# Kernel optimization log

Hardware: AMD Instinct MI355X
Metric: run time of the kernel (lower is better)

The kernel has to match this reference:

```python
import jax, jax.numpy as jnp
import numpy as np

# Module hyperparameters (from init_kwargs)
IN_C = 64
OUT_C = 64
K = 3
STRIDE = 1
PAD = 1
DIL = 1
OVERLAP = 4
CENTER_SIZE = 4

# Input sizes
B, H, W = 16, 128, 128


def _crop_mask(h, w):
    """Static (trace-time) crop mask: zeros on the central crop window, ones elsewhere.

    Matches the intended semantics of CropConv's python-loop mask: rows
    [crop_start, crop_start+crop_size) x cols [crop_start, crop_start+crop_size)
    of the HxW output grid are zeroed.
    """
    crop_start = (h - h // CENTER_SIZE) // 2 - OVERLAP  # 44 for h=128
    crop_size = h // CENTER_SIZE + 2 * OVERLAP          # 40 for h=128
    m = np.ones((h, w), dtype=np.float32)
    m[crop_start:crop_start + crop_size, crop_start:crop_start + crop_size] = 0.0
    return jnp.asarray(m)


def setup_inputs() -> dict:
    key = jax.random.key(0)
    kx, kw = jax.random.split(key)
    x = jax.random.normal(kx, (B, IN_C, H, W), dtype=jnp.float32)
    # kaiming_normal_ fan_out init: std = sqrt(2 / (out_channels * k * k))
    w_std = np.sqrt(2.0 / (OUT_C * K * K)).astype(np.float32)
    weight = jax.random.normal(kw, (OUT_C, IN_C, K, K), dtype=jnp.float32) * w_std
    return {"x": x, "weight": weight}


def reference(x, weight):
    # im2col (Unfold) + matmul == a standard dense conv; use the fused conv primitive.
    out = jax.lax.conv_general_dilated(
        x, weight,
        window_strides=(STRIDE, STRIDE),
        padding=((PAD, PAD), (PAD, PAD)),
        rhs_dilation=(DIL, DIL),
        dimension_numbers=("NCHW", "OIHW", "NCHW"),
    )  # [B, OUT_C, H, W] (same-size conv)
    mask = _crop_mask(out.shape[2], out.shape[3])  # [H, W], {0,1}
    # torch.where(mask, out, 0) == out * mask (mask is constant wrt grads)
    return out * mask
```

## Files before the change

kernel.cpp:

```cpp
#include <hip/hip_runtime.h>
#include <stdint.h>


#define B_ 16
#define C_ 64
#define H_ 128
#define W_ 128

#define TCOLS_A 130
#define XLDS_A (3 * TCOLS_A * 8)

typedef float f32x4 __attribute__((ext_vector_type(4)));
typedef short bf16x8 __attribute__((ext_vector_type(8)));

__device__ inline unsigned short f2bf(float f) {
    union { float f; uint32_t u; } v; v.f = f;
    uint32_t u = v.u + 0x7FFF + ((v.u >> 16) & 1);
    return (unsigned short)(u >> 16);
}

__global__ __launch_bounds__(256) void xform_weight(
    const float* __restrict__ wgt, uint16_t* __restrict__ Wb)
{
    int L = blockIdx.x * 256 + threadIdx.x;
    int e    = L & 7;
    int lane = (L >> 3) & 63;
    int i    = (L >> 9) & 3;
    int ch   = (L >> 11) & 1;
    int kk   = L >> 12;
    int oc   = i * 16 + (lane & 15);
    int ic   = ch * 32 + (lane >> 4) * 8 + e;
    Wb[L] = f2bf(wgt[((size_t)oc * 64 + ic) * 9 + kk]);
}

__global__ __launch_bounds__(256, 2) void conv_main(
    const uint4* __restrict__ Wq,
    const float* __restrict__ x,
    float* __restrict__ out)
{
    __shared__ uint4 lds[XLDS_A];

    const int t    = threadIdx.x;
    const int lane = t & 63;
    const int wv   = t >> 6;
    const int n    = lane & 15;
    const int q    = lane >> 4;

    const int d    = blockIdx.x;
    const int orig = (d & 7) * 256 + (d >> 3);
    const int ht   = orig & 127;
    const int b    = orig >> 7;

    const int ohalf = wv & 1;
    const int wq    = (wv >> 1) * 64;

    bf16x8 Areg[18][2];
    #pragma unroll
    for (int g = 0; g < 18; ++g)
        #pragma unroll
        for (int i = 0; i < 2; ++i)
            Areg[g][i] = __builtin_bit_cast(bf16x8,
                Wq[(g * 4 + ohalf * 2 + i) * 64 + lane]);

    {
        const int j     = t & 7;
        const int c4    = t >> 3;
        const int cbase = 1 + c4 * 4;
        const int wg0   = c4 * 4;

        #pragma unroll
        for (int r = 0; r < 3; ++r) {
            const int h = ht - 1 + r;
            if (h < 0 || h >= H_) {
                uint4 z; z.x = z.y = z.z = z.w = 0;
                #pragma unroll
                for (int cc = 0; cc < 4; ++cc)
                    lds[(r * TCOLS_A + cbase + cc) * 8 +
                        ((j + cbase + cc) & 7)] = z;
            } else {
                const float* src =
                    x + (((size_t)(b * C_ + j * 8)) * H_ + h) * W_ + wg0;
                f32x4 f[8];
                #pragma unroll
                for (int e = 0; e < 8; ++e)
                    f[e] = *(const f32x4*)(src + (size_t)e * (H_ * W_));
                #pragma unroll
                for (int cc = 0; cc < 4; ++cc) {
                    uint32_t u[4];
                    #pragma unroll
                    for (int p = 0; p < 4; ++p)
                        u[p] = (uint32_t)f2bf(f[2 * p][cc]) |
                               ((uint32_t)f2bf(f[2 * p + 1][cc]) << 16);
                    lds[(r * TCOLS_A + cbase + cc) * 8 +
                        ((j + cbase + cc) & 7)] = *(const uint4*)u;
                }
            }
        }
        if (t < 48) {
            const int ce = (t < 24) ? 0 : (TCOLS_A - 1);
            const int u  = (t < 24) ? t : t - 24;
            const int r  = u >> 3, jj = u & 7;
            uint4 z; z.x = z.y = z.z = z.w = 0;
            lds[(r * TCOLS_A + ce) * 8 + ((jj + ce) & 7)] = z;
        }
    }
    __syncthreads();

    f32x4 acc[2][4];
    #pragma unroll
    for (int i = 0; i < 2; ++i)
        #pragma unroll
        for (int f = 0; f < 4; ++f)
            acc[i][f] = (f32x4){0.f, 0.f, 0.f, 0.f};

    #pragma unroll
    for (int kh = 0; kh < 3; ++kh) {
        #pragma unroll
        for (int kw = 0; kw < 3; ++kw) {
            #pragma unroll
            for (int ch = 0; ch < 2; ++ch) {
                const int g = (kh * 3 + kw) * 2 + ch;
                bf16x8 bb[4];
                #pragma unroll
                for (int f = 0; f < 4; ++f) {
                    const int ct  = wq + f * 16 + n + kw;
                    const int idx = (kh * TCOLS_A + ct) * 8 +
                                    ((ch * 4 + q + ct) & 7);
                    bb[f] = __builtin_bit_cast(bf16x8, lds[idx]);
                }
                #pragma unroll
                for (int i = 0; i < 2; ++i)
                    #pragma unroll
                    for (int f = 0; f < 4; ++f)
                        acc[i][f] = __builtin_amdgcn_mfma_f32_16x16x32_bf16(
                            Areg[g][i], bb[f], acc[i][f], 0, 0, 0);
            }
        }
    }

    const int  h  = ht;
    const bool hz = (h >= 44 && h < 84);
    #pragma unroll
    for (int f = 0; f < 4; ++f) {
        const int w0 = wq + f * 16 + n;
        const bool zz = hz && (w0 >= 44 && w0 < 84);
        #pragma unroll
        for (int i = 0; i < 2; ++i) {
            #pragma unroll
            for (int r = 0; r < 4; ++r) {
                const int oc = ohalf * 32 + i * 16 + q * 4 + r;
                out[(((size_t)b * C_ + oc) * H_ + h) * W_ + w0] =
                    zz ? 0.f : acc[i][f][r];
            }
        }
    }
}

#define WLDS_U4 4608
#define FXLDS_U4 4096

__global__ __launch_bounds__(256, 1) void conv_fused(
    const float* __restrict__ x,
    const float* __restrict__ wgt,
    float* __restrict__ out)
{
    __shared__ uint4 lds[WLDS_U4 + FXLDS_U4];
    uint16_t* lds16 = (uint16_t*)lds;

    const int t    = threadIdx.x;
    const int lane = t & 63;
    const int wv   = t >> 6;
    const int n    = lane & 15;
    const int q    = lane >> 4;

    const int d    = blockIdx.x;
    const int orig = (d & 7) * 128 + (d >> 3);
    const int b    = orig >> 6;
    const int h0   = (orig & 63) * 2;

    #pragma unroll
    for (int p = 0; p < 2; ++p) {
        const int a_  = t + 256 * p;
        const int oc  = a_ >> 3;
        const int oct = a_ & 7;
        const float* src = wgt + (size_t)oc * 576 + (size_t)oct * 72;
        f32x4 w4[18];
        #pragma unroll
        for (int j = 0; j < 18; ++j) w4[j] = ((const f32x4*)src)[j];
        const int ch = oct >> 2, qq = oct & 3;
        const int ii = oc >> 4,  nn = oc & 15;
        #pragma unroll
        for (int kk = 0; kk < 9; ++kk) {
            #define WELEM(e) ((uint32_t)f2bf(w4[((e)*9 + kk) >> 2][((e)*9 + kk) & 3]))
            uint4 val;
            val.x = WELEM(0) | (WELEM(1) << 16);
            val.y = WELEM(2) | (WELEM(3) << 16);
            val.z = WELEM(4) | (WELEM(5) << 16);
            val.w = WELEM(6) | (WELEM(7) << 16);
            #undef WELEM
            lds[((kk * 2 + ch) * 4 + ii) * 64 + qq * 16 + nn] = val;
        }
    }

    {
        const int ic    = t >> 2;
        const int w0    = (t & 3) * 32;
        const int jslot = ic >> 3;
        const int esub  = ic & 7;
        #pragma unroll
        for (int r = 0; r < 4; ++r) {
            const int h = h0 - 1 + r;
            if (h < 0 || h >= H_) {
                uint4 z; z.x = z.y = z.z = z.w = 0;
                #pragma unroll
                for (int k = 0; k < 4; ++k)
                    lds[WLDS_U4 + r * 1024 + k * 256 + t] = z;
            } else {
                const float* src =
                    x + (((size_t)(b * C_ + ic)) * H_ + h) * W_ + w0;
                f32x4 v4[8];
                #pragma unroll
                for (int j = 0; j < 8; ++j) v4[j] = ((const f32x4*)src)[j];
                #pragma unroll
                for (int k = 0; k < 32; ++k) {
                    const int c    = w0 + k;
                    const int slot = (jslot + c) & 7;
                    lds16[WLDS_U4 * 8 + ((r * 128 + c) * 8 + slot) * 8 + esub] =
                        f2bf(v4[k >> 2][k & 3]);
                }
            }
        }
    }
    __syncthreads();

    f32x4 acc[4][4];
    #pragma unroll
    for (int i = 0; i < 4; ++i)
        #pragma unroll
        for (int tt = 0; tt < 4; ++tt)
            acc[i][tt] = (f32x4){0.f, 0.f, 0.f, 0.f};

    const int wb = (wv & 1) * 64;
    const uint4* Wl = lds;
    const uint4* Xl = lds + WLDS_U4;
    const bool lz = (wb + n) == 0;
    const bool rz = (wb + n) == 79;
    const bf16x8 zfrag = 0;

    #pragma unroll
    for (int kh = 0; kh < 3; ++kh) {
        const int row = (wv >> 1) + kh;
        #pragma unroll
        for (int kw = 0; kw < 3; ++kw) {
            const int kk = kh * 3 + kw;
            #pragma unroll
            for (int ch = 0; ch < 2; ++ch) {
                bf16x8 a[4], bb[4];
                #pragma unroll
                for (int i = 0; i < 4; ++i)
                    a[i] = __builtin_bit_cast(bf16x8,
                        Wl[((kk * 2 + ch) * 4 + i) * 64 + lane]);
                #pragma unroll
                for (int tt = 0; tt < 4; ++tt) {
                    int c   = wb + tt * 16 + n + kw - 1;
                    int cc  = min(max(c, 0), 127);
                    int idx = (row * 128 + cc) * 8 + ((ch * 4 + q + cc) & 7);
                    bf16x8 v = __builtin_bit_cast(bf16x8, Xl[idx]);
                    if (kw == 0 && tt == 0) v = lz ? zfrag : v;
                    if (kw == 2 && tt == 3) v = rz ? zfrag : v;
                    bb[tt] = v;
                }
                #pragma unroll
                for (int i = 0; i < 4; ++i)
                    #pragma unroll
                    for (int tt = 0; tt < 4; ++tt)
                        acc[i][tt] = __builtin_amdgcn_mfma_f32_16x16x32_bf16(
                            a[i], bb[tt], acc[i][tt], 0, 0, 0);
            }
        }
    }

    const int  h  = h0 + (wv >> 1);
    const bool hz = (h >= 44 && h < 84);
    #pragma unroll
    for (int i = 0; i < 4; ++i) {
        #pragma unroll
        for (int tt = 0; tt < 4; ++tt) {
            const int  w0 = wb + tt * 16 + n;
            const bool zz = hz && (w0 >= 44 && w0 < 84);
            #pragma unroll
            for (int r = 0; r < 4; ++r) {
                const int oc = i * 16 + q * 4 + r;
                out[(((size_t)b * C_ + oc) * H_ + h) * W_ + w0] =
                    zz ? 0.f : acc[i][tt][r];
            }
        }
    }
}

extern "C" void kernel_launch(void* const* d_in, const int* in_sizes, int n_in,
                              void* d_out, int out_size, void* d_ws, size_t ws_size,
                              hipStream_t stream) {
    const float* x   = (const float*)d_in[0];
    const float* wgt = (const float*)d_in[1];
    float* out       = (float*)d_out;

    const size_t W_BYTES = 9 * 2 * 4 * 64 * 16;
    if (ws_size >= W_BYTES) {
        uint16_t* Wb = (uint16_t*)d_ws;
        xform_weight<<<dim3(144), dim3(256), 0, stream>>>(wgt, Wb);
        conv_main<<<dim3(2048), dim3(256), 0, stream>>>(
            (const uint4*)Wb, x, out);
    } else {
        conv_fused<<<dim3(1024), dim3(256), 0, stream>>>(x, wgt, out);
    }
}
```

Measured before the change: 138.9 us.

## Process four output rows per block with a rotating LDS row ring and prefetch

Each block now computes four consecutive output rows instead of one, keeping a 4-slot ring of input rows in LDS so each new row needs only one extra row load instead of three. The next row's global loads are issued before the MFMA loop and written to LDS afterwards, overlapping memory latency with compute. This reduces redundant input reads and weight register reloads, but cuts the grid from 2048 to 512 blocks, which lowers parallelism and occupancy slack, and adds per-iteration barriers.

```diff
diff --git a/kernel.cpp b/kernel.cpp
--- a/kernel.cpp
+++ b/kernel.cpp
@@ -8,7 +8,9 @@
 #define W_ 128
 
 #define TCOLS_A 130
-#define XLDS_A (3 * TCOLS_A * 8)
+#define ROWU4   (TCOLS_A * 8)
+#define XLDS_R  (4 * ROWU4)
+#define T_TILES 4
 
 typedef float f32x4 __attribute__((ext_vector_type(4)));
 typedef short bf16x8 __attribute__((ext_vector_type(8)));
@@ -33,12 +35,51 @@
     Wb[L] = f2bf(wgt[((size_t)oc * 64 + ic) * 9 + kk]);
 }
 
+__device__ __forceinline__ void stage_row_now(
+    uint4* lds, const float* __restrict__ xb, int p, int t)
+{
+    const int j     = t & 7;
+    const int c4    = t >> 3;
+    const int cbase = 1 + c4 * 4;
+    const int wg0   = c4 * 4;
+    const int sb    = (p & 3) * ROWU4;
+    const int h     = p - 1;
+    if (h < 0 || h >= H_) {
+        uint4 z; z.x = z.y = z.z = z.w = 0;
+        #pragma unroll
+        for (int cc = 0; cc < 4; ++cc)
+            lds[sb + (cbase + cc) * 8 + ((j + cbase + cc) & 7)] = z;
+    } else {
+        const float* src = xb + ((size_t)(j * 8) * H_ + h) * W_ + wg0;
+        f32x4 f[8];
+        #pragma unroll
+        for (int e = 0; e < 8; ++e)
+            f[e] = *(const f32x4*)(src + (size_t)e * (H_ * W_));
+        #pragma unroll
+        for (int cc = 0; cc < 4; ++cc) {
+            uint32_t u[4];
+            #pragma unroll
+            for (int pp = 0; pp < 4; ++pp)
+                u[pp] = (uint32_t)f2bf(f[2 * pp][cc]) |
+                        ((uint32_t)f2bf(f[2 * pp + 1][cc]) << 16);
+            lds[sb + (cbase + cc) * 8 + ((j + cbase + cc) & 7)] =
+                *(const uint4*)u;
+        }
+    }
+    if (t < 16) {
+        const int ce = (t < 8) ? 0 : (TCOLS_A - 1);
+        const int jj = t & 7;
+        uint4 z; z.x = z.y = z.z = z.w = 0;
+        lds[sb + ce * 8 + ((jj + ce) & 7)] = z;
+    }
+}
+
 __global__ __launch_bounds__(256, 2) void conv_main(
     const uint4* __restrict__ Wq,
     const float* __restrict__ x,
     float* __restrict__ out)
 {
-    __shared__ uint4 lds[XLDS_A];
+    __shared__ uint4 lds[XLDS_R];
 
     const int t    = threadIdx.x;
     const int lane = t & 63;
@@ -47,12 +88,15 @@
     const int q    = lane >> 4;
 
     const int d    = blockIdx.x;
-    const int orig = (d & 7) * 256 + (d >> 3);
-    const int ht   = orig & 127;
-    const int b    = orig >> 7;
+    const int orig = (d & 7) * 64 + (d >> 3);
+    const int hg   = orig & 31;
+    const int b    = orig >> 5;
+    const int h0   = hg * 4;
 
     const int ohalf = wv & 1;
     const int wq    = (wv >> 1) * 64;
+
+    const float* xb = x + (size_t)b * C_ * H_ * W_;
 
     bf16x8 Areg[18][2];
     #pragma unroll
@@ -62,95 +106,109 @@
             Areg[g][i] = __builtin_bit_cast(bf16x8,
                 Wq[(g * 4 + ohalf * 2 + i) * 64 + lane]);
 
-    {
-        const int j     = t & 7;
-        const int c4    = t >> 3;
-        const int cbase = 1 + c4 * 4;
-        const int wg0   = c4 * 4;
-
-        #pragma unroll
-        for (int r = 0; r < 3; ++r) {
-            const int h = ht - 1 + r;
-            if (h < 0 || h >= H_) {
-                uint4 z; z.x = z.y = z.z = z.w = 0;
-                #pragma unroll
-                for (int cc = 0; cc < 4; ++cc)
-                    lds[(r * TCOLS_A + cbase + cc) * 8 +
-                        ((j + cbase + cc) & 7)] = z;
-            } else {
-                const float* src =
-                    x + (((size_t)(b * C_ + j * 8)) * H_ + h) * W_ + wg0;
-                f32x4 f[8];
-                #pragma unroll
-                for (int e = 0; e < 8; ++e)
-                    f[e] = *(const f32x4*)(src + (size_t)e * (H_ * W_));
+    #pragma unroll
+    for (int r = 0; r < 3; ++r)
+        stage_row_now(lds, xb, h0 + r, t);
+
+    const int sj    = t & 7;
+    const int sc4   = t >> 3;
+    const int scb   = 1 + sc4 * 4;
+    const int swg0  = sc4 * 4;
+
+    #pragma unroll 1
+    for (int it = 0; it < T_TILES; ++it) {
+        const int ht = h0 + it;
+        __syncthreads();
+
+        const int  pnext = ht + 3;
+        const bool dopf  = (it < T_TILES - 1);
+        const bool zrow  = (pnext - 1 >= H_);
+        f32x4 pf[8];
+        if (dopf && !zrow) {
+            const float* src =
+                xb + ((size_t)(sj * 8) * H_ + (pnext - 1)) * W_ + swg0;
+            #pragma unroll
+            for (int e = 0; e < 8; ++e)
+                pf[e] = *(const f32x4*)(src + (size_t)e * (H_ * W_));
+        }
+        __builtin_amdgcn_sched_barrier(0);
+
+        f32x4 acc[2][4];
+        #pragma unroll
+        for (int i = 0; i < 2; ++i)
+            #pragma unroll
+            for (int f = 0; f < 4; ++f)
+                acc[i][f] = (f32x4){0.f, 0.f, 0.f, 0.f};
+
+        const int sbs[3] = { (ht & 3) * ROWU4,
+                             ((ht + 1) & 3) * ROWU4,
+                             ((ht + 2) & 3) * ROWU4 };
+
+        #pragma unroll
+        for (int kh = 0; kh < 3; ++kh) {
+            #pragma unroll
+            for (int kw = 0; kw < 3; ++kw) {
+                #pragma unroll
+                for (int ch = 0; ch < 2; ++ch) {
+                    const int g = (kh * 3 + kw) * 2 + ch;
+                    bf16x8 bb[4];
+                    #pragma unroll
+                    for (int f = 0; f < 4; ++f) {
+                        const int ct  = wq + f * 16 + n + kw;
+                        const int idx = sbs[kh] + ct * 8 +
+                                        ((ch * 4 + q + ct) & 7);
+                        bb[f] = __builtin_bit_cast(bf16x8, lds[idx]);
+                    }
+                    #pragma unroll
+                    for (int i = 0; i < 2; ++i)
+                        #pragma unroll
+                        for (int f = 0; f < 4; ++f)
+                            acc[i][f] = __builtin_amdgcn_mfma_f32_16x16x32_bf16(
+                                Areg[g][i], bb[f], acc[i][f], 0, 0, 0);
+                }
+            }
+        }
+
+        if (dopf) {
+            const int sb = (pnext & 3) * ROWU4;
+            if (!zrow) {
                 #pragma unroll
                 for (int cc = 0; cc < 4; ++cc) {
                     uint32_t u[4];
                     #pragma unroll
-                    for (int p = 0; p < 4; ++p)
-                        u[p] = (uint32_t)f2bf(f[2 * p][cc]) |
-                               ((uint32_t)f2bf(f[2 * p + 1][cc]) << 16);
-                    lds[(r * TCOLS_A + cbase + cc) * 8 +
-                        ((j + cbase + cc) & 7)] = *(const uint4*)u;
-                }
-            }
-        }
-        if (t < 48) {
-            const int ce = (t < 24) ? 0 : (TCOLS_A - 1);
-            const int u  = (t < 24) ? t : t - 24;
-            const int r  = u >> 3, jj = u & 7;
-            uint4 z; z.x = z.y = z.z = z.w = 0;
-            lds[(r * TCOLS_A + ce) * 8 + ((jj + ce) & 7)] = z;
-        }
-    }
-    __syncthreads();
-
-    f32x4 acc[2][4];
-    #pragma unroll
-    for (int i = 0; i < 2; ++i)
-        #pragma unroll
-        for (int f = 0; f < 4; ++f)
-            acc[i][f] = (f32x4){0.f, 0.f, 0.f, 0.f};
-
-    #pragma unroll
-    for (int kh = 0; kh < 3; ++kh) {
-        #pragma unroll
-        for (int kw = 0; kw < 3; ++kw) {
-            #pragma unroll
-            for (int ch = 0; ch < 2; ++ch) {
-                const int g = (kh * 3 + kw) * 2 + ch;
-                bf16x8 bb[4];
-                #pragma unroll
-                for (int f = 0; f < 4; ++f) {
-                    const int ct  = wq + f * 16 + n + kw;
-                    const int idx = (kh * TCOLS_A + ct) * 8 +
-                                    ((ch * 4 + q + ct) & 7);
-                    bb[f] = __builtin_bit_cast(bf16x8, lds[idx]);
-                }
-                #pragma unroll
-                for (int i = 0; i < 2; ++i)
-                    #pragma unroll
-                    for (int f = 0; f < 4; ++f)
-                        acc[i][f] = __builtin_amdgcn_mfma_f32_16x16x32_bf16(
-                            Areg[g][i], bb[f], acc[i][f], 0, 0, 0);
-            }
-        }
-    }
-
-    const int  h  = ht;
-    const bool hz = (h >= 44 && h < 84);
-    #pragma unroll
-    for (int f = 0; f < 4; ++f) {
-        const int w0 = wq + f * 16 + n;
-        const bool zz = hz && (w0 >= 44 && w0 < 84);
-        #pragma unroll
-        for (int i = 0; i < 2; ++i) {
-            #pragma unroll
-            for (int r = 0; r < 4; ++r) {
-                const int oc = ohalf * 32 + i * 16 + q * 4 + r;
-                out[(((size_t)b * C_ + oc) * H_ + h) * W_ + w0] =
-                    zz ? 0.f : acc[i][f][r];
+                    for (int pp = 0; pp < 4; ++pp)
+                        u[pp] = (uint32_t)f2bf(pf[2 * pp][cc]) |
+                                ((uint32_t)f2bf(pf[2 * pp + 1][cc]) << 16);
+                    lds[sb + (scb + cc) * 8 + ((sj + scb + cc) & 7)] =
+                        *(const uint4*)u;
+                }
+            } else {
+                uint4 z; z.x = z.y = z.z = z.w = 0;
+                #pragma unroll
+                for (int cc = 0; cc < 4; ++cc)
+                    lds[sb + (scb + cc) * 8 + ((sj + scb + cc) & 7)] = z;
+            }
+            if (t < 16) {
+                const int ce = (t < 8) ? 0 : (TCOLS_A - 1);
+                const int jj = t & 7;
+                uint4 z; z.x = z.y = z.z = z.w = 0;
+                lds[sb + ce * 8 + ((jj + ce) & 7)] = z;
+            }
+        }
+
+        const bool hz = (ht >= 44 && ht < 84);
+        #pragma unroll
+        for (int f = 0; f < 4; ++f) {
+            const int w0 = wq + f * 16 + n;
+            const bool zz = hz && (w0 >= 44 && w0 < 84);
+            #pragma unroll
+            for (int i = 0; i < 2; ++i) {
+                #pragma unroll
+                for (int r = 0; r < 4; ++r) {
+                    const int oc = ohalf * 32 + i * 16 + q * 4 + r;
+                    out[(((size_t)b * C_ + oc) * H_ + ht) * W_ + w0] =
+                        zz ? 0.f : acc[i][f][r];
+                }
             }
         }
     }
@@ -309,7 +367,7 @@
     if (ws_size >= W_BYTES) {
         uint16_t* Wb = (uint16_t*)d_ws;
         xform_weight<<<dim3(144), dim3(256), 0, stream>>>(wgt, Wb);
-        conv_main<<<dim3(2048), dim3(256), 0, stream>>>(
+        conv_main<<<dim3(512), dim3(256), 0, stream>>>(
             (const uint4*)Wb, x, out);
     } else {
         conv_fused<<<dim3(1024), dim3(256), 0, stream>>>(x, wgt, out);
```

New measurement: 140.9 us. About the same (+1.5%).
